# Performance work log

Hardware: AMD Instinct MI355X
Metric: run time of the kernel (lower is better)

## Reference

```python
import jax, jax.numpy as jnp
import numpy as np

B, L, C = 32, 4096, 64
PL, PC = 64, 16          # patch sizes along L and C
NP = 256                 # num_patches
OUT = 512                # output_dim
FS = 1000.0              # sampling frequency -> T = 1/FS


def setup_inputs() -> dict:
    key = jax.random.key(0)
    ks = jax.random.split(key, 7)
    d_in = PL * (PC * 2)
    return {
        "x": jax.random.normal(ks[0], (B, L, C), dtype=jnp.float32),
        "start_L": jax.random.randint(ks[1], (B, NP), 0, L - PL + 1, dtype=jnp.int32),
        "start_C": jax.random.randint(ks[2], (B, NP), 0, C - PC + 1, dtype=jnp.int32),
        "w1": jax.random.normal(ks[3], (OUT, d_in), dtype=jnp.float32) / np.sqrt(d_in),
        "b1": jax.random.normal(ks[4], (OUT,), dtype=jnp.float32) * 0.01,
        "w2": jax.random.normal(ks[5], (OUT, OUT), dtype=jnp.float32) / np.sqrt(OUT),
        "b2": jax.random.normal(ks[6], (OUT,), dtype=jnp.float32) * 0.01,
    }


def reference(x, start_L, start_C, w1, b1, w2, b2):
    T = 1.0 / FS
    t = jnp.arange(L, dtype=jnp.float32) * T                      # [L]

    # patch index grids (wrapping, as in the torch module)
    idx_L = (start_L[:, :, None] + jnp.arange(PL, dtype=jnp.int32)) % L   # [B,NP,PL]
    idx_C = (start_C[:, :, None] + jnp.arange(PC, dtype=jnp.int32)) % C   # [B,NP,PC]

    # double gather: patches[b,p,i,j] = x[b, idx_L[b,p,i], idx_C[b,p,j]]
    b_idx = jnp.arange(B, dtype=jnp.int32)[:, None, None, None]
    patches = x[b_idx, idx_L[:, :, :, None], idx_C[:, :, None, :]]        # [B,NP,PL,PC]

    # time embedding gathered with the same L indices, broadcast over PC
    t_patches = jnp.broadcast_to(t[idx_L][:, :, :, None], (B, NP, PL, PC))

    feats = jnp.concatenate([patches, t_patches], axis=-1)                # [B,NP,PL,2*PC]
    feats = feats.reshape(B, NP, PL * 2 * PC)

    h = jnp.einsum('bpd,od->bpo', feats, w1) + b1
    h = jax.nn.silu(h)
    out = jnp.einsum('bpo,qo->bpq', h, w2) + b2                           # [B,NP,OUT]
    return out
```

## Files before the change

### kernel.cpp

```cpp
#include <hip/hip_runtime.h>
#include <hip/hip_bf16.h>
#include <stdint.h>

#define LL   4096
#define CCH  64
#define DOUT 512
#define MM   8192
#define TT   0.001f

using bf16 = __hip_bfloat16;
typedef __attribute__((ext_vector_type(8))) short bf16x8;
typedef __attribute__((ext_vector_type(4))) float f32x4;

__device__ __forceinline__ void async_copy16(void* lds, const void* g) {
    __builtin_amdgcn_global_load_lds(
        (const __attribute__((address_space(1))) void*)g,
        (__attribute__((address_space(3))) void*)lds,
        16, 0, 0);
}

__device__ __forceinline__ uint2 pack4_bf16(float a, float b, float c, float d) {
    union { bf16 h[4]; uint2 u; } p;
    p.h[0] = __float2bfloat16(a);
    p.h[1] = __float2bfloat16(b);
    p.h[2] = __float2bfloat16(c);
    p.h[3] = __float2bfloat16(d);
    return p.u;
}

__global__ __launch_bounds__(256) void prep(
    const float* __restrict__ w1, const float* __restrict__ b1,
    const float* __restrict__ w2,
    bf16* __restrict__ w1p, bf16* __restrict__ w2p,
    float* __restrict__ A1, float* __restrict__ C1)
{
    const int blk = blockIdx.x;
    if (blk < 512) {
        int g   = blk * 256 + threadIdx.x;
        int kk0 = (g & 15) * 4;
        int col = (g >> 4) & 511;
        int it  = g >> 13;
        float4 v = *(const float4*)(w1 + (size_t)col * 2048
                                    + (it * 4 + (kk0 >> 4)) * 32 + (kk0 & 15));
        int off = (it * 512 + col) * 64 + (((kk0 >> 3) ^ (col & 7)) * 8) + (kk0 & 7);
        *(uint2*)(w1p + off) = pack4_bf16(v.x, v.y, v.z, v.w);
    } else if (blk < 768) {
        int g   = (blk - 512) * 256 + threadIdx.x;
        int kk0 = (g & 15) * 4;
        int col = (g >> 4) & 511;
        int it2 = g >> 13;
        float4 v = *(const float4*)(w2 + (size_t)col * 512 + it2 * 64 + kk0);
        int off = (it2 * 512 + col) * 64 + (((kk0 >> 3) ^ (col & 7)) * 8) + (kk0 & 7);
        *(uint2*)(w2p + off) = pack4_bf16(v.x, v.y, v.z, v.w);
    } else {
        const int o = (blk - 768) * 4 + (threadIdx.x >> 6);
        const int l = threadIdx.x & 63;
        const float* wr = w1 + (size_t)o * 2048 + l * 32 + 16;
        float s0 = 0.f;
#pragma unroll
        for (int j = 0; j < 16; ++j) s0 += wr[j];
        float s1 = (float)l * s0;
#pragma unroll
        for (int off = 32; off > 0; off >>= 1) {
            s0 += __shfl_down(s0, off);
            s1 += __shfl_down(s1, off);
        }
        if (l == 0) {
            A1[o] = TT * s0;
            C1[o] = b1[o] + TT * s1;
        }
    }
}

__global__ __launch_bounds__(512, 2) void mega(
    const float* __restrict__ x, const int* __restrict__ sLg,
    const int* __restrict__ sCg, const bf16* __restrict__ w1p,
    const bf16* __restrict__ w2p, const float* __restrict__ A1,
    const float* __restrict__ C1, const float* __restrict__ b2,
    float* __restrict__ out)
{
    __shared__ __align__(16) char smem_raw[139264];
    bf16* const Bs0 = (bf16*)smem_raw;
    bf16* const Bs1 = (bf16*)(smem_raw + 65536);
    bf16* const As0 = (bf16*)(smem_raw + 131072);
    bf16* const As1 = (bf16*)(smem_raw + 135168);
    bf16* const Hs  = (bf16*)(smem_raw + 65536);

    const int t    = threadIdx.x;
    const int lane = t & 63;
    const int wave = t >> 6;
    const int fr   = lane & 15;
    const int fq   = lane >> 4;
    const int m0   = blockIdx.x * 32;
    const int b    = m0 >> 8;

    const int gr  = t >> 4;
    const int gs  = t & 15;
    const int gsl = sLg[m0 + gr];
    const int gsc = sCg[m0 + gr];
    const float* gx = x + ((size_t)b * LL + gsl + (gs >> 2)) * CCH + gsc + (gs & 3) * 4;
    const int aoff = gr * 64 + (((gs >> 1) ^ (gr & 7)) * 8) + (gs & 1) * 4;

    const bf16* bsrc1 = w1p + (size_t)t * 8;
    const bf16* bsrc2 = w2p + (size_t)t * 8;
    const int   wu8   = wave * 64 * 8;

    f32x4 acc[2][4] = {};

    {
#pragma unroll
        for (int c = 0; c < 8; ++c)
            async_copy16(Bs0 + c * 4096 + wu8, bsrc1 + c * 4096);
        float4 v = *(const float4*)gx;
        *(uint2*)(As0 + aoff) = pack4_bf16(v.x, v.y, v.z, v.w);
    }
    float4 xv = *(const float4*)(gx + 4 * CCH);

    for (int it = 0; it < 16; ++it) {
        __syncthreads();
        bf16* const Bc = (it & 1) ? Bs1 : Bs0;
        bf16* const Ac = (it & 1) ? As1 : As0;
        if (it < 15) {
            bf16* const Bn = (it & 1) ? Bs0 : Bs1;
            bf16* const An = (it & 1) ? As0 : As1;
            const bf16* bs = bsrc1 + (size_t)(it + 1) * 32768;
#pragma unroll
            for (int c = 0; c < 8; ++c)
                async_copy16(Bn + c * 4096 + wu8, bs + c * 4096);
            *(uint2*)(An + aoff) = pack4_bf16(xv.x, xv.y, xv.z, xv.w);
            const int itn = (it + 2 < 16) ? (it + 2) : 15;
            xv = *(const float4*)(gx + (size_t)itn * 4 * CCH);
        }

        bf16x8 af[2][2], bfr[4][2];
#pragma unroll
        for (int i = 0; i < 2; ++i)
#pragma unroll
            for (int ks = 0; ks < 2; ++ks)
                af[i][ks] = *(const bf16x8*)&Ac[(i * 16 + fr) * 64
                                + (((ks * 4 + fq) ^ (fr & 7)) * 8)];
#pragma unroll
        for (int j = 0; j < 4; ++j)
#pragma unroll
            for (int ks = 0; ks < 2; ++ks)
                bfr[j][ks] = *(const bf16x8*)&Bc[(wave * 64 + j * 16 + fr) * 64
                                + (((ks * 4 + fq) ^ (fr & 7)) * 8)];
#pragma unroll
        for (int ks = 0; ks < 2; ++ks)
#pragma unroll
            for (int i = 0; i < 2; ++i)
#pragma unroll
                for (int j = 0; j < 4; ++j)
                    acc[i][j] = __builtin_amdgcn_mfma_f32_16x16x32_bf16(
                        af[i][ks], bfr[j][ks], acc[i][j], 0, 0, 0);
    }
    __syncthreads();

#pragma unroll
    for (int c = 0; c < 8; ++c)
        async_copy16(Bs0 + c * 4096 + wu8, bsrc2 + c * 4096);

    {
        float slr[2][4];
#pragma unroll
        for (int i = 0; i < 2; ++i)
#pragma unroll
            for (int rr = 0; rr < 4; ++rr)
                slr[i][rr] = (float)sLg[m0 + i * 16 + fq * 4 + rr];
#pragma unroll
        for (int j = 0; j < 4; ++j) {
            const int col = wave * 64 + j * 16 + fr;
            const float av = A1[col];
            const float cv = C1[col];
            const int c8 = col >> 3, c7 = col & 7;
#pragma unroll
            for (int i = 0; i < 2; ++i)
#pragma unroll
                for (int rr = 0; rr < 4; ++rr) {
                    const int row = i * 16 + fq * 4 + rr;
                    float v = acc[i][j][rr] + slr[i][rr] * av + cv;
                    v = v / (1.0f + __expf(-v));
                    Hs[row * 512 + ((c8 ^ (row & 7)) * 8) + c7] = __float2bfloat16(v);
                }
        }
    }

    f32x4 acc2[2][4] = {};
    for (int it2 = 0; it2 < 8; ++it2) {
        __syncthreads();
        bf16x8 af[2][2], bfr[4][2];
#pragma unroll
        for (int i = 0; i < 2; ++i)
#pragma unroll
            for (int ks = 0; ks < 2; ++ks) {
                const int row = i * 16 + fr;
                af[i][ks] = *(const bf16x8*)&Hs[row * 512
                                + (((it2 * 8 + ks * 4 + fq) ^ (row & 7)) * 8)];
            }
#pragma unroll
        for (int j = 0; j < 4; ++j)
#pragma unroll
            for (int ks = 0; ks < 2; ++ks)
                bfr[j][ks] = *(const bf16x8*)&Bs0[(wave * 64 + j * 16 + fr) * 64
                                + (((ks * 4 + fq) ^ (fr & 7)) * 8)];
        __syncthreads();
        if (it2 < 7) {
            const bf16* bs = bsrc2 + (size_t)(it2 + 1) * 32768;
#pragma unroll
            for (int c = 0; c < 8; ++c)
                async_copy16(Bs0 + c * 4096 + wu8, bs + c * 4096);
        }
#pragma unroll
        for (int ks = 0; ks < 2; ++ks)
#pragma unroll
            for (int i = 0; i < 2; ++i)
#pragma unroll
                for (int j = 0; j < 4; ++j)
                    acc2[i][j] = __builtin_amdgcn_mfma_f32_16x16x32_bf16(
                        af[i][ks], bfr[j][ks], acc2[i][j], 0, 0, 0);
    }

#pragma unroll
    for (int j = 0; j < 4; ++j) {
        const int col = wave * 64 + j * 16 + fr;
        const float bv = b2[col];
#pragma unroll
        for (int i = 0; i < 2; ++i)
#pragma unroll
            for (int rr = 0; rr < 4; ++rr) {
                const int row = m0 + i * 16 + fq * 4 + rr;
                out[(size_t)row * 512 + col] = acc2[i][j][rr] + bv;
            }
    }
}

extern "C" void kernel_launch(void* const* d_in, const int* in_sizes, int n_in,
                              void* d_out, int out_size, void* d_ws, size_t ws_size,
                              hipStream_t stream)
{
    const float* x  = (const float*)d_in[0];
    const int*   sL = (const int*)  d_in[1];
    const int*   sC = (const int*)  d_in[2];
    const float* w1 = (const float*)d_in[3];
    const float* b1 = (const float*)d_in[4];
    const float* w2 = (const float*)d_in[5];
    const float* b2 = (const float*)d_in[6];
    float* out = (float*)d_out;

    char* ws = (char*)d_ws;
    bf16*  w1p = (bf16*)ws;
    bf16*  w2p = (bf16*)(ws + (1 << 20));
    float* A1  = (float*)(ws + (1 << 20) + (1 << 19));
    float* C1  = A1 + DOUT;

    prep<<<896, 256, 0, stream>>>(w1, b1, w2, w1p, w2p, A1, C1);
    mega<<<MM / 32, 512, 0, stream>>>(x, sL, sC, w1p, w2p, A1, C1, b2, out);
}
```

Before: 129.0 us.

## Load weight fragments directly from global into registers, stage whole patch tile in LDS

```diff
diff --git a/kernel.cpp b/kernel.cpp
--- a/kernel.cpp
+++ b/kernel.cpp
@@ -11,13 +11,6 @@
 using bf16 = __hip_bfloat16;
 typedef __attribute__((ext_vector_type(8))) short bf16x8;
 typedef __attribute__((ext_vector_type(4))) float f32x4;
-
-__device__ __forceinline__ void async_copy16(void* lds, const void* g) {
-    __builtin_amdgcn_global_load_lds(
-        (const __attribute__((address_space(1))) void*)g,
-        (__attribute__((address_space(3))) void*)lds,
-        16, 0, 0);
-}
 
 __device__ __forceinline__ uint2 pack4_bf16(float a, float b, float c, float d) {
     union { bf16 h[4]; uint2 u; } p;
@@ -31,27 +24,28 @@
 __global__ __launch_bounds__(256) void prep(
     const float* __restrict__ w1, const float* __restrict__ b1,
     const float* __restrict__ w2,
-    bf16* __restrict__ w1p, bf16* __restrict__ w2p,
+    bf16* __restrict__ w1g, bf16* __restrict__ w2g,
     float* __restrict__ A1, float* __restrict__ C1)
 {
     const int blk = blockIdx.x;
     if (blk < 512) {
         int g   = blk * 256 + threadIdx.x;
-        int kk0 = (g & 15) * 4;
-        int col = (g >> 4) & 511;
-        int it  = g >> 13;
-        float4 v = *(const float4*)(w1 + (size_t)col * 2048
-                                    + (it * 4 + (kk0 >> 4)) * 32 + (kk0 & 15));
-        int off = (it * 512 + col) * 64 + (((kk0 >> 3) ^ (col & 7)) * 8) + (kk0 & 7);
-        *(uint2*)(w1p + off) = pack4_bf16(v.x, v.y, v.z, v.w);
+        int kk0 = (g & 7) * 4;
+        int col = (g >> 3) & 511;
+        int ic  = g >> 12;
+        int l   = ic * 2 + (kk0 >> 4);
+        int j0  = kk0 & 15;
+        float4 v = *(const float4*)(w1 + (size_t)col * 2048 + l * 32 + j0);
+        *(uint2*)(w1g + ((size_t)(ic * 512 + col) * 32 + kk0)) =
+            pack4_bf16(v.x, v.y, v.z, v.w);
     } else if (blk < 768) {
         int g   = (blk - 512) * 256 + threadIdx.x;
-        int kk0 = (g & 15) * 4;
-        int col = (g >> 4) & 511;
-        int it2 = g >> 13;
-        float4 v = *(const float4*)(w2 + (size_t)col * 512 + it2 * 64 + kk0);
-        int off = (it2 * 512 + col) * 64 + (((kk0 >> 3) ^ (col & 7)) * 8) + (kk0 & 7);
-        *(uint2*)(w2p + off) = pack4_bf16(v.x, v.y, v.z, v.w);
+        int kk0 = (g & 7) * 4;
+        int col = (g >> 3) & 511;
+        int ic2 = g >> 12;
+        float4 v = *(const float4*)(w2 + (size_t)col * 512 + ic2 * 32 + kk0);
+        *(uint2*)(w2g + ((size_t)(ic2 * 512 + col) * 32 + kk0)) =
+            pack4_bf16(v.x, v.y, v.z, v.w);
     } else {
         const int o = (blk - 768) * 4 + (threadIdx.x >> 6);
         const int l = threadIdx.x & 63;
@@ -74,17 +68,13 @@
 
 __global__ __launch_bounds__(512, 2) void mega(
     const float* __restrict__ x, const int* __restrict__ sLg,
-    const int* __restrict__ sCg, const bf16* __restrict__ w1p,
-    const bf16* __restrict__ w2p, const float* __restrict__ A1,
+    const int* __restrict__ sCg, const bf16* __restrict__ w1g,
+    const bf16* __restrict__ w2g, const float* __restrict__ A1,
     const float* __restrict__ C1, const float* __restrict__ b2,
     float* __restrict__ out)
 {
-    __shared__ __align__(16) char smem_raw[139264];
-    bf16* const Bs0 = (bf16*)smem_raw;
-    bf16* const Bs1 = (bf16*)(smem_raw + 65536);
-    bf16* const As0 = (bf16*)(smem_raw + 131072);
-    bf16* const As1 = (bf16*)(smem_raw + 135168);
-    bf16* const Hs  = (bf16*)(smem_raw + 65536);
+    __shared__ __align__(16) bf16 Asm[32 * 1024];
+    bf16* const Hs = Asm;
 
     const int t    = threadIdx.x;
     const int lane = t & 63;
@@ -94,71 +84,61 @@
     const int m0   = blockIdx.x * 32;
     const int b    = m0 >> 8;
 
-    const int gr  = t >> 4;
-    const int gs  = t & 15;
-    const int gsl = sLg[m0 + gr];
-    const int gsc = sCg[m0 + gr];
-    const float* gx = x + ((size_t)b * LL + gsl + (gs >> 2)) * CCH + gsc + (gs & 3) * 4;
-    const int aoff = gr * 64 + (((gs >> 1) ^ (gr & 7)) * 8) + (gs & 1) * 4;
-
-    const bf16* bsrc1 = w1p + (size_t)t * 8;
-    const bf16* bsrc2 = w2p + (size_t)t * 8;
-    const int   wu8   = wave * 64 * 8;
-
+    {
+        const int gr  = t >> 4;
+        const int gs  = t & 15;
+        const int gsl = sLg[m0 + gr];
+        const int gsc = sCg[m0 + gr];
+        const float* gx = x + ((size_t)b * LL + gsl + (gs >> 2)) * CCH
+                            + gsc + (gs & 3) * 4;
+        float4 xv[16];
+#pragma unroll
+        for (int p = 0; p < 16; ++p)
+            xv[p] = *(const float4*)(gx + (size_t)p * 4 * CCH);
+#pragma unroll
+        for (int p = 0; p < 16; ++p) {
+            const int l = 4 * p + (gs >> 2);
+            const int u = l * 2 + ((gs & 3) >> 1);
+            const int idx = gr * 1024 + ((u ^ (gr & 7)) * 8) + (gs & 1) * 4;
+            *(uint2*)(Asm + idx) = pack4_bf16(xv[p].x, xv[p].y, xv[p].z, xv[p].w);
+        }
+    }
+    __syncthreads();
+
+    const bf16* const w1base = w1g + (size_t)(wave * 64 + fr) * 32 + fq * 8;
     f32x4 acc[2][4] = {};
-
-    {
-#pragma unroll
-        for (int c = 0; c < 8; ++c)
-            async_copy16(Bs0 + c * 4096 + wu8, bsrc1 + c * 4096);
-        float4 v = *(const float4*)gx;
-        *(uint2*)(As0 + aoff) = pack4_bf16(v.x, v.y, v.z, v.w);
-    }
-    float4 xv = *(const float4*)(gx + 4 * CCH);
-
-    for (int it = 0; it < 16; ++it) {
-        __syncthreads();
-        bf16* const Bc = (it & 1) ? Bs1 : Bs0;
-        bf16* const Ac = (it & 1) ? As1 : As0;
-        if (it < 15) {
-            bf16* const Bn = (it & 1) ? Bs0 : Bs1;
-            bf16* const An = (it & 1) ? As0 : As1;
-            const bf16* bs = bsrc1 + (size_t)(it + 1) * 32768;
-#pragma unroll
-            for (int c = 0; c < 8; ++c)
-                async_copy16(Bn + c * 4096 + wu8, bs + c * 4096);
-            *(uint2*)(An + aoff) = pack4_bf16(xv.x, xv.y, xv.z, xv.w);
-            const int itn = (it + 2 < 16) ? (it + 2) : 15;
-            xv = *(const float4*)(gx + (size_t)itn * 4 * CCH);
-        }
-
-        bf16x8 af[2][2], bfr[4][2];
-#pragma unroll
-        for (int i = 0; i < 2; ++i)
-#pragma unroll
-            for (int ks = 0; ks < 2; ++ks)
-                af[i][ks] = *(const bf16x8*)&Ac[(i * 16 + fr) * 64
-                                + (((ks * 4 + fq) ^ (fr & 7)) * 8)];
+    {
+        bf16x8 bnx[4];
 #pragma unroll
         for (int j = 0; j < 4; ++j)
-#pragma unroll
-            for (int ks = 0; ks < 2; ++ks)
-                bfr[j][ks] = *(const bf16x8*)&Bc[(wave * 64 + j * 16 + fr) * 64
-                                + (((ks * 4 + fq) ^ (fr & 7)) * 8)];
-#pragma unroll
-        for (int ks = 0; ks < 2; ++ks)
+            bnx[j] = *(const bf16x8*)(w1base + j * 512);
+#pragma unroll
+        for (int it = 0; it < 32; ++it) {
+            bf16x8 bcur[4];
+#pragma unroll
+            for (int j = 0; j < 4; ++j) bcur[j] = bnx[j];
+            if (it < 31) {
+                const bf16* p = w1base + (size_t)(it + 1) * 16384;
+#pragma unroll
+                for (int j = 0; j < 4; ++j)
+                    bnx[j] = *(const bf16x8*)(p + j * 512);
+            }
+            bf16x8 af[2];
+#pragma unroll
+            for (int i = 0; i < 2; ++i) {
+                const int row = i * 16 + fr;
+                const int u   = it * 4 + fq;
+                af[i] = *(const bf16x8*)&Asm[row * 1024 + ((u ^ (row & 7)) * 8)];
+            }
 #pragma unroll
             for (int i = 0; i < 2; ++i)
 #pragma unroll
                 for (int j = 0; j < 4; ++j)
                     acc[i][j] = __builtin_amdgcn_mfma_f32_16x16x32_bf16(
-                        af[i][ks], bfr[j][ks], acc[i][j], 0, 0, 0);
+                        af[i], bcur[j], acc[i][j], 0, 0, 0);
+        }
     }
     __syncthreads();
-
-#pragma unroll
-    for (int c = 0; c < 8; ++c)
-        async_copy16(Bs0 + c * 4096 + wu8, bsrc2 + c * 4096);
 
     {
         float slr[2][4];
@@ -184,40 +164,40 @@
                 }
         }
     }
-
+    __syncthreads();
+
+    const bf16* const w2base = w2g + (size_t)(wave * 64 + fr) * 32 + fq * 8;
     f32x4 acc2[2][4] = {};
-    for (int it2 = 0; it2 < 8; ++it2) {
-        __syncthreads();
-        bf16x8 af[2][2], bfr[4][2];
-#pragma unroll
-        for (int i = 0; i < 2; ++i)
-#pragma unroll
-            for (int ks = 0; ks < 2; ++ks) {
+    {
+        bf16x8 bnx[4];
+#pragma unroll
+        for (int j = 0; j < 4; ++j)
+            bnx[j] = *(const bf16x8*)(w2base + j * 512);
+#pragma unroll
+        for (int it2 = 0; it2 < 16; ++it2) {
+            bf16x8 bcur[4];
+#pragma unroll
+            for (int j = 0; j < 4; ++j) bcur[j] = bnx[j];
+            if (it2 < 15) {
+                const bf16* p = w2base + (size_t)(it2 + 1) * 16384;
+#pragma unroll
+                for (int j = 0; j < 4; ++j)
+                    bnx[j] = *(const bf16x8*)(p + j * 512);
+            }
+            bf16x8 af[2];
+#pragma unroll
+            for (int i = 0; i < 2; ++i) {
                 const int row = i * 16 + fr;
-                af[i][ks] = *(const bf16x8*)&Hs[row * 512
-                                + (((it2 * 8 + ks * 4 + fq) ^ (row & 7)) * 8)];
-            }
-#pragma unroll
-        for (int j = 0; j < 4; ++j)
-#pragma unroll
-            for (int ks = 0; ks < 2; ++ks)
-                bfr[j][ks] = *(const bf16x8*)&Bs0[(wave * 64 + j * 16 + fr) * 64
-                                + (((ks * 4 + fq) ^ (fr & 7)) * 8)];
-        __syncthreads();
-        if (it2 < 7) {
-            const bf16* bs = bsrc2 + (size_t)(it2 + 1) * 32768;
-#pragma unroll
-            for (int c = 0; c < 8; ++c)
-                async_copy16(Bs0 + c * 4096 + wu8, bs + c * 4096);
-        }
-#pragma unroll
-        for (int ks = 0; ks < 2; ++ks)
+                const int u2  = it2 * 4 + fq;
+                af[i] = *(const bf16x8*)&Hs[row * 512 + ((u2 ^ (row & 7)) * 8)];
+            }
 #pragma unroll
             for (int i = 0; i < 2; ++i)
 #pragma unroll
                 for (int j = 0; j < 4; ++j)
                     acc2[i][j] = __builtin_amdgcn_mfma_f32_16x16x32_bf16(
-                        af[i][ks], bfr[j][ks], acc2[i][j], 0, 0, 0);
+                        af[i], bcur[j], acc2[i][j], 0, 0, 0);
+        }
     }
 
 #pragma unroll
@@ -248,11 +228,11 @@
     float* out = (float*)d_out;
 
     char* ws = (char*)d_ws;
-    bf16*  w1p = (bf16*)ws;
-    bf16*  w2p = (bf16*)(ws + (1 << 20));
+    bf16*  w1g = (bf16*)ws;
+    bf16*  w2g = (bf16*)(ws + (1 << 20));
     float* A1  = (float*)(ws + (1 << 20) + (1 << 19));
     float* C1  = A1 + DOUT;
 
-    prep<<<896, 256, 0, stream>>>(w1, b1, w2, w1p, w2p, A1, C1);
-    mega<<<MM / 32, 512, 0, stream>>>(x, sL, sC, w1p, w2p, A1, C1, b2, out);
-}
+    prep<<<896, 256, 0, stream>>>(w1, b1, w2, w1g, w2g, A1, C1);
+    mega<<<MM / 32, 512, 0, stream>>>(x, sL, sC, w1g, w2g, A1, C1, b2, out);
+}
```

Result: faster. 123.8 us (-4.0%).
